# Optimization experiments

Measured on AMD Instinct MI355X. Metric: run time of the kernel, lower is better.

The kernel has to match this reference:

```python
import jax, jax.numpy as jnp
import numpy as np

N = 50000   # nodes per node type
D = 256     # in_dim == out_dim
H = 8       # num heads
DK = D // H # 32
E = 500000  # edges per edge type
LN_EPS = 1e-5


def setup_inputs() -> dict:
    key = jax.random.key(0)
    ks = jax.random.split(key, 16)
    w = lambda k, shape: jax.random.normal(k, shape, dtype=jnp.float32) * 0.05
    xav = np.sqrt(6.0 / (DK + DK))
    return {
        'feats': jax.random.normal(ks[0], (2, N, D), dtype=jnp.float32),
        'Wk': w(ks[1], (2, D, D)), 'bk': jnp.zeros((2, D), jnp.float32),
        'Wq': w(ks[2], (2, D, D)), 'bq': jnp.zeros((2, D), jnp.float32),
        'Wv': w(ks[3], (2, D, D)), 'bv': jnp.zeros((2, D), jnp.float32),
        'Wa': w(ks[4], (2, D, D)), 'ba': jnp.zeros((2, D), jnp.float32),
        'ln_w': jnp.ones((2, D), jnp.float32), 'ln_b': jnp.zeros((2, D), jnp.float32),
        'skip': jnp.ones((2,), jnp.float32),
        'mu': jnp.ones((2, H), jnp.float32),
        'w_att': jax.random.uniform(ks[5], (2, H, DK, DK), jnp.float32, -xav, xav),
        'w_msg': jax.random.uniform(ks[6], (2, H, DK, DK), jnp.float32, -xav, xav),
        'src': jax.random.randint(ks[7], (2, E), 0, N, dtype=jnp.int32),
        'dst': jax.random.randint(ks[8], (2, E), 0, N, dtype=jnp.int32),
    }


def _edge_softmax(scores, seg, n):
    # scores: (E, H); softmax over edges sharing the same destination node
    m = jax.ops.segment_max(scores, seg, num_segments=n)          # (N, H)
    e = jnp.exp(scores - m[seg])
    s = jax.ops.segment_sum(e, seg, num_segments=n)               # (N, H)
    return e / s[seg]


def _forward(feats, Wk, bk, Wq, bq, Wv, bv, Wa, ba, ln_w, ln_b, skip,
             mu, w_att, w_msg, src, dst):
    # canonical etypes: 0 = author->paper, 1 = paper->author
    stypes, dtypes = (0, 1), (1, 0)
    scale = 1.0 / jnp.sqrt(jnp.asarray(DK, feats.dtype))
    h = [None, None]
    for et in range(2):
        st, dt = stypes[et], dtypes[et]
        s_idx, d_idx = src[et], dst[et]
        k = (feats[st] @ Wk[st] + bk[st]).reshape(N, H, DK)
        k = jnp.einsum('nhi,hij->nhj', k, w_att[et])
        v = (feats[st] @ Wv[st] + bv[st]).reshape(N, H, DK)
        v = jnp.einsum('nhi,hij->nhj', v, w_msg[et])
        q = (feats[dt] @ Wq[dt] + bq[dt]).reshape(N, H, DK)
        t = jnp.einsum('ehd,ehd->eh', q[d_idx], k[s_idx])         # (E, H)
        attn = _edge_softmax(t * mu[et] * scale, d_idx, N)        # (E, H)
        msg = v[s_idx] * attn[..., None]                          # (E, H, DK)
        h[dt] = jax.ops.segment_sum(msg, d_idx, num_segments=N).reshape(N, D)
    h = jnp.stack(h)  # (2, N, D); each ntype receives from exactly one etype

    trans = jnp.einsum('tnd,tde->tne', h, Wa) + ba[:, None, :]
    alpha = jax.nn.sigmoid(skip)[:, None, None]
    out = alpha * trans + (1.0 - alpha) * feats
    mean = out.mean(-1, keepdims=True)
    var = out.var(-1, keepdims=True)
    out = (out - mean) * jax.lax.rsqrt(var + LN_EPS)
    return out * ln_w[:, None, :] + ln_b[:, None, :]


def reference(feats, Wk, bk, Wq, bq, Wv, bv, Wa, ba, ln_w, ln_b, skip,
              mu, w_att, w_msg, src, dst):
    return _forward(feats, Wk, bk, Wq, bq, Wv, bv, Wa, ba, ln_w, ln_b, skip,
                    mu, w_att, w_msg, src, dst)
```

## Files before the change

kernel.cpp:

```cpp
#include <hip/hip_runtime.h>
#include <hip/hip_bf16.h>

#define D 256
#define H 8
#define DK 32

typedef unsigned short ushort_t;
typedef unsigned int uint_t;
typedef __attribute__((ext_vector_type(4))) float floatx4;
typedef __attribute__((ext_vector_type(2))) float floatx2;
typedef __attribute__((ext_vector_type(8))) short shortx8;
typedef __attribute__((ext_vector_type(8))) unsigned short ushortx8;

typedef __attribute__((address_space(3))) void lds_void_t;
typedef const __attribute__((address_space(1))) void gbl_void_t;

__device__ __forceinline__ float b2f(ushort_t u) {
    return __uint_as_float(((uint_t)u) << 16);
}
__device__ __forceinline__ floatx2 b2x2(uint_t u) {
    floatx2 r;
    r.x = __uint_as_float(u << 16);
    r.y = __uint_as_float(u & 0xffff0000u);
    return r;
}
__device__ __forceinline__ ushort_t f2b(float f) {
    uint_t u = __float_as_uint(f);
    uint_t r = (u + 0x7FFFu + ((u >> 16) & 1u)) >> 16;
    return (ushort_t)r;
}
__device__ __forceinline__ void async_cp16(const void* g, void* l) {
    __builtin_amdgcn_global_load_lds((gbl_void_t*)g, (lds_void_t*)l, 16, 0, 0);
}

__global__ void cvt_bf16(const float* __restrict__ in, ushort_t* __restrict__ out, size_t n4) {
    size_t i = (size_t)blockIdx.x * blockDim.x + threadIdx.x;
    if (i >= n4) return;
    float4 v = ((const float4*)in)[i];
    ushort4 o;
    o.x = f2b(v.x); o.y = f2b(v.y); o.z = f2b(v.z); o.w = f2b(v.w);
    ((ushort4*)out)[i] = o;
}

__global__ void zero_int(int* __restrict__ p, int n) {
    int i = blockIdx.x * blockDim.x + threadIdx.x;
    if (i < n) p[i] = 0;
}

__global__ void fold_weights(const float* __restrict__ Wk, const float* __restrict__ bk,
                             const float* __restrict__ Wv, const float* __restrict__ bv,
                             const float* __restrict__ w_att, const float* __restrict__ w_msg,
                             float* __restrict__ Wkc, float* __restrict__ bkc,
                             float* __restrict__ Wvc, float* __restrict__ bvc) {
    int r = blockIdx.x, et = blockIdx.y, which = blockIdx.z;
    int tid = threadIdx.x;
    const float* Wsrc = (which ? Wv : Wk) + (size_t)et * D * D + (size_t)r * D;
    const float* wt   = (which ? w_msg : w_att) + (size_t)et * H * DK * DK;
    float* Wdst = (which ? Wvc : Wkc) + (size_t)et * D * D;
    __shared__ float wrow[D];
    wrow[tid] = Wsrc[tid];
    __syncthreads();
    int h = tid >> 5, j = tid & 31;
    const float* wth = wt + h * DK * DK;
    float acc = 0.f;
#pragma unroll 8
    for (int i = 0; i < DK; i++) acc += wrow[h * 32 + i] * wth[i * 32 + j];
    Wdst[(size_t)r * D + tid] = acc;
    if (r == 0) {
        const float* bsrc = (which ? bv : bk) + et * D;
        float* bdst = (which ? bvc : bkc) + et * D;
        float bacc = 0.f;
#pragma unroll 8
        for (int i = 0; i < DK; i++) bacc += bsrc[h * 32 + i] * wth[i * 32 + j];
        bdst[tid] = bacc;
    }
}

__global__ void pack_weights(const float* __restrict__ Wq, const float* __restrict__ bq,
                             const float* __restrict__ Wkc, const float* __restrict__ bkc,
                             const float* __restrict__ Wvc, const float* __restrict__ bvc,
                             const float* __restrict__ Wa,
                             ushort_t* __restrict__ WT_all, ushort_t* __restrict__ WaT,
                             float* __restrict__ bias_all) {
    int idx = blockIdx.x * blockDim.x + threadIdx.x;
    const int NW = 2 * 768 * 256;
    if (idx < NW) {
        int t = idx / (768 * 256);
        int rem = idx - t * 768 * 256;
        int n = rem >> 8, k = rem & 255;
        int sec = n >> 8, nn = n & 255;
        const float* W = (sec == 0) ? Wq : (sec == 1) ? Wkc : Wvc;
        WT_all[idx] = f2b(W[(size_t)t * D * D + (size_t)k * D + nn]);
    } else if (idx < NW + 2 * 256 * 256) {
        int r = idx - NW;
        int t = r / (256 * 256);
        int rem = r - t * 256 * 256;
        int n = rem >> 8, k = rem & 255;
        WaT[r] = f2b(Wa[(size_t)t * D * D + (size_t)k * D + n]);
    }
    if (idx < 2 * 768) {
        int t = idx / 768, n = idx % 768;
        int sec = n >> 8, nn = n & 255;
        const float* b = (sec == 0) ? bq : (sec == 1) ? bkc : bvc;
        bias_all[idx] = b[t * D + nn];
    }
}

#define TM 128
#define TN 128
#define TKK 32
__launch_bounds__(256)
__global__ void gemm_mfma(const ushort_t* __restrict__ A, int lda,
                          const ushort_t* __restrict__ BT,
                          const float* __restrict__ bias,
                          ushort_t* __restrict__ C, int ldc, int M) {
    __shared__ ushort_t As[TM * TKK];
    __shared__ ushort_t Bs[TN * TKK];
    int tid = threadIdx.x;
    int w = tid >> 6, lane = tid & 63;

    int nwg  = gridDim.x * gridDim.y;
    int orig = blockIdx.y * gridDim.x + blockIdx.x;
    int q = nwg >> 3, r = nwg & 7;
    int xcd = orig & 7, loc = orig >> 3;
    int wgid = (xcd < r ? xcd * (q + 1) : r * (q + 1) + (xcd - r) * q) + loc;
    int ncol = gridDim.y;
    int rowt = wgid / ncol;
    int colt = wgid - rowt * ncol;
    int bm = rowt * TM;
    int bn = colt * TN;

    int wm = (w & 1) * 64, wn = (w >> 1) * 64;

    floatx4 acc[4][4] = {};

    int srow = lane >> 2;
    int scol = (lane & 3) * 8;

    for (int kc = 0; kc < 256; kc += TKK) {
#pragma unroll
        for (int j = 0; j < 2; j++) {
            int rr = w * 32 + j * 16;
            int gr = bm + rr + srow; if (gr >= M) gr = M - 1;
            async_cp16(A + (size_t)gr * lda + kc + scol, As + rr * TKK);
            int gn = bn + rr + srow;
            async_cp16(BT + (size_t)gn * 256 + kc + scol, Bs + rr * TKK);
        }
        __builtin_amdgcn_s_waitcnt(0x0F70);
        __syncthreads();

        int fr = lane & 15, fq = lane >> 4;
        shortx8 af[4], bf[4];
#pragma unroll
        for (int i = 0; i < 4; i++)
            af[i] = *(const shortx8*)(As + (wm + i * 16 + fr) * TKK + fq * 8);
#pragma unroll
        for (int j = 0; j < 4; j++)
            bf[j] = *(const shortx8*)(Bs + (wn + j * 16 + fr) * TKK + fq * 8);
#pragma unroll
        for (int i = 0; i < 4; i++)
#pragma unroll
            for (int j = 0; j < 4; j++)
                acc[i][j] = __builtin_amdgcn_mfma_f32_16x16x32_bf16(af[i], bf[j], acc[i][j], 0, 0, 0);
        __syncthreads();
    }

    int fr = lane & 15, fq = lane >> 4;
#pragma unroll
    for (int i = 0; i < 4; i++) {
#pragma unroll
        for (int j = 0; j < 4; j++) {
            int col = bn + wn + j * 16 + fr;
            float bv = bias[col];
#pragma unroll
            for (int rr = 0; rr < 4; rr++) {
                int row = bm + wm + i * 16 + fq * 4 + rr;
                if (row < M) C[(size_t)row * ldc + col] = f2b(acc[i][j][rr] + bv);
            }
        }
    }
}

__global__ void count_deg(const int* __restrict__ dst, int* __restrict__ deg,
                          int N, int E) {
    int i = blockIdx.x * blockDim.x + threadIdx.x;
    if (i >= 2 * E) return;
    int et = i / E, e = i - et * E;
    int d = dst[(size_t)et * E + e];
    atomicAdd(&deg[(1 - et) * N + d], 1);
}

__launch_bounds__(256)
__global__ void scan_blocks(int* __restrict__ deg, int* __restrict__ bsum, int n) {
    __shared__ int wsum[4];
    int tid = threadIdx.x, lane = tid & 63, w = tid >> 6;
    int i = blockIdx.x * 256 + tid;
    int v = (i < n) ? deg[i] : 0;
    int x = v;
#pragma unroll
    for (int off = 1; off < 64; off <<= 1) {
        int y = __shfl_up(x, off);
        if (lane >= off) x += y;
    }
    if (lane == 63) wsum[w] = x;
    __syncthreads();
    int add = 0;
    if (w > 0) add += wsum[0];
    if (w > 1) add += wsum[1];
    if (w > 2) add += wsum[2];
    int incl = x + add;
    if (i < n) deg[i] = incl - v;
    if (tid == 255) bsum[blockIdx.x] = incl;
}

__launch_bounds__(512)
__global__ void scan_tops(int* __restrict__ bsum, int* __restrict__ row_ptr,
                          int nb, int n) {
    __shared__ int wsum[8];
    int tid = threadIdx.x, lane = tid & 63, w = tid >> 6;
    int v = (tid < nb) ? bsum[tid] : 0;
    int x = v;
#pragma unroll
    for (int off = 1; off < 64; off <<= 1) {
        int y = __shfl_up(x, off);
        if (lane >= off) x += y;
    }
    if (lane == 63) wsum[w] = x;
    __syncthreads();
    int add = 0;
    for (int j = 0; j < w; j++) add += wsum[j];
    int incl = x + add;
    if (tid < nb) bsum[tid] = incl - v;
    if (tid == nb - 1) row_ptr[n] = incl;
}

__launch_bounds__(256)
__global__ void scan_apply(const int* __restrict__ excl, const int* __restrict__ bsum,
                           int* __restrict__ row_ptr, int* __restrict__ cursor, int n) {
    int i = blockIdx.x * 256 + threadIdx.x;
    if (i >= n) return;
    int e = excl[i] + bsum[blockIdx.x];
    row_ptr[i] = e;
    cursor[i] = e;
}

__global__ void fill_edges(const int* __restrict__ src, const int* __restrict__ dst,
                           int* __restrict__ cursor, int* __restrict__ ebuf,
                           int N, int E) {
    int i = blockIdx.x * blockDim.x + threadIdx.x;
    if (i >= 2 * E) return;
    int et = i / E, e = i - et * E;
    int d = dst[(size_t)et * E + e];
    int s = src[(size_t)et * E + e];
    int pos = atomicAdd(&cursor[(1 - et) * N + d], 1);
    ebuf[pos] = s;
}

__launch_bounds__(256)
__global__ void node_aggregate(ushort_t* __restrict__ QKV, const float* __restrict__ mu,
                               const int* __restrict__ row_ptr, const int* __restrict__ ebuf,
                               int N) {
    int wid = (blockIdx.x * blockDim.x + threadIdx.x) >> 6;
    int lane = threadIdx.x & 63;
    if (wid >= 2 * N) return;
    int dt = (wid >= N) ? 1 : 0;
    int et = 1 - dt;
    int l = lane & 31;
    int half = lane >> 5;
    int h = l >> 2;

    uint4 qu = ((const uint4*)(QKV + (size_t)wid * 768))[l];
    floatx2 q01 = b2x2(qu.x), q23 = b2x2(qu.y), q45 = b2x2(qu.z), q67 = b2x2(qu.w);
    float sc = mu[et * H + h] * 0.17677669529663687f;
    int beg = row_ptr[wid], end = row_ptr[wid + 1];
    const ushort_t* KVb = QKV + (size_t)et * N * 768;

    floatx2 a01 = {0.f, 0.f}, a23 = {0.f, 0.f}, a45 = {0.f, 0.f}, a67 = {0.f, 0.f};
    float ssum = 0.f;

    int idx = beg + half;
    uint4 ku0 = {}, vu0 = {};
    int s1v = 0;
    if (idx < end) {
        int s0v = ebuf[idx];
        int i2 = idx + 2;
        s1v = ebuf[i2 < end ? i2 : idx];
        const ushort_t* srow = KVb + (size_t)s0v * 768 + l * 8;
        ku0 = *(const uint4*)(srow + 256);
        vu0 = *(const uint4*)(srow + 512);
    }
    while (idx < end) {
        int i2 = idx + 2;
        uint4 ku1 = ku0, vu1 = vu0;
        int s2v = s1v;
        if (i2 < end) {
            int i4 = idx + 4;
            s2v = ebuf[i4 < end ? i4 : i2];
            const ushort_t* srow = KVb + (size_t)s1v * 768 + l * 8;
            ku1 = *(const uint4*)(srow + 256);
            vu1 = *(const uint4*)(srow + 512);
        }
        floatx2 pv = q01 * b2x2(ku0.x);
        pv += q23 * b2x2(ku0.y);
        pv += q45 * b2x2(ku0.z);
        pv += q67 * b2x2(ku0.w);
        float p = pv.x + pv.y;
        p += __shfl_xor(p, 1);
        p += __shfl_xor(p, 2);
        float ex = __expf(p * sc);
        ssum += ex;
        floatx2 ex2 = {ex, ex};
        a01 += ex2 * b2x2(vu0.x);
        a23 += ex2 * b2x2(vu0.y);
        a45 += ex2 * b2x2(vu0.z);
        a67 += ex2 * b2x2(vu0.w);
        ku0 = ku1; vu0 = vu1; s1v = s2v;
        idx = i2;
    }
    ssum += __shfl_xor(ssum, 32);
    a01.x += __shfl_xor(a01.x, 32); a01.y += __shfl_xor(a01.y, 32);
    a23.x += __shfl_xor(a23.x, 32); a23.y += __shfl_xor(a23.y, 32);
    a45.x += __shfl_xor(a45.x, 32); a45.y += __shfl_xor(a45.y, 32);
    a67.x += __shfl_xor(a67.x, 32); a67.y += __shfl_xor(a67.y, 32);
    float r = (ssum > 0.f) ? 1.0f / ssum : 0.0f;
    if (half == 0) {
        ushortx8 hv;
        hv[0] = f2b(a01.x * r); hv[1] = f2b(a01.y * r);
        hv[2] = f2b(a23.x * r); hv[3] = f2b(a23.y * r);
        hv[4] = f2b(a45.x * r); hv[5] = f2b(a45.y * r);
        hv[6] = f2b(a67.x * r); hv[7] = f2b(a67.y * r);
        ((ushortx8*)(QKV + (size_t)wid * 768))[l] = hv;
    }
}

__launch_bounds__(256)
__global__ void skip_ln(const ushort_t* __restrict__ trans, const float* __restrict__ feats,
                        const float* __restrict__ lnw, const float* __restrict__ lnb,
                        const float* __restrict__ skip, float* __restrict__ out, int N) {
    int wid = (blockIdx.x * blockDim.x + threadIdx.x) >> 6;
    int lane = threadIdx.x & 63;
    if (wid >= 2 * N) return;
    int t = (wid >= N) ? 1 : 0;
    float alpha = 1.0f / (1.0f + __expf(-skip[t]));
    float beta = 1.0f - alpha;
    size_t base = (size_t)wid * D;
    ushort4 tu = ((const ushort4*)(trans + base))[lane];
    float4 fu = ((const float4*)(feats + base))[lane];
    float x0 = alpha * b2f(tu.x) + beta * fu.x;
    float x1 = alpha * b2f(tu.y) + beta * fu.y;
    float x2 = alpha * b2f(tu.z) + beta * fu.z;
    float x3 = alpha * b2f(tu.w) + beta * fu.w;
    float s  = x0 + x1 + x2 + x3;
    float sq = x0 * x0 + x1 * x1 + x2 * x2 + x3 * x3;
#pragma unroll
    for (int off = 1; off < 64; off <<= 1) {
        s  += __shfl_xor(s,  off);
        sq += __shfl_xor(sq, off);
    }
    float mean = s * (1.0f / 256.0f);
    float var  = sq * (1.0f / 256.0f) - mean * mean;
    float r = rsqrtf(var + 1e-5f);
    float4 w4 = ((const float4*)(lnw + t * D))[lane];
    float4 b4 = ((const float4*)(lnb + t * D))[lane];
    float4 o;
    o.x = (x0 - mean) * r * w4.x + b4.x;
    o.y = (x1 - mean) * r * w4.y + b4.y;
    o.z = (x2 - mean) * r * w4.z + b4.z;
    o.w = (x3 - mean) * r * w4.w + b4.w;
    ((float4*)(out + base))[lane] = o;
}

extern "C" void kernel_launch(void* const* d_in, const int* in_sizes, int n_in,
                              void* d_out, int out_size, void* d_ws, size_t ws_size,
                              hipStream_t stream) {
    const float* feats = (const float*)d_in[0];
    const float* Wk    = (const float*)d_in[1];
    const float* bk    = (const float*)d_in[2];
    const float* Wq    = (const float*)d_in[3];
    const float* bq    = (const float*)d_in[4];
    const float* Wv    = (const float*)d_in[5];
    const float* bv    = (const float*)d_in[6];
    const float* Wa    = (const float*)d_in[7];
    const float* ba    = (const float*)d_in[8];
    const float* ln_w  = (const float*)d_in[9];
    const float* ln_b  = (const float*)d_in[10];
    const float* skip  = (const float*)d_in[11];
    const float* mu    = (const float*)d_in[12];
    const float* w_att = (const float*)d_in[13];
    const float* w_msg = (const float*)d_in[14];
    const int*   src   = (const int*)d_in[15];
    const int*   dst   = (const int*)d_in[16];
    float* out = (float*)d_out;

    const int N = in_sizes[0] / (2 * D);
    const int E = in_sizes[15] / 2;
    const int NN = 2 * N;
    const size_t ND2 = 2 * (size_t)N * D;

    float* ws = (float*)d_ws;
    size_t off = 0;
    float* Wkc  = ws + off; off += 2 * (size_t)D * D;
    float* Wvc  = ws + off; off += 2 * (size_t)D * D;
    float* bkc  = ws + off; off += 2 * D;
    float* bvc  = ws + off; off += 2 * D;
    float* bias_all = ws + off; off += 2 * 768;
    ushort_t* WT_all = (ushort_t*)(ws + off); off += 2 * 768 * 256 / 2;
    ushort_t* WaT    = (ushort_t*)(ws + off); off += 2 * 256 * 256 / 2;
    ushort_t* featsb = (ushort_t*)(ws + off); off += ND2 / 2;
    ushort_t* QKV    = (ushort_t*)(ws + off); off += 2 * (size_t)N * 768 / 2;
    int* deg     = (int*)(ws + off); off += NN;
    int* row_ptr = (int*)(ws + off); off += NN + 1;
    int* cursor  = (int*)(ws + off); off += NN + 1;
    int* ebuf    = (int*)(ws + off); off += 2 * (size_t)E;
    int* bsum    = (int*)(ws + off); off += 512;

    const int nb = (NN + 255) / 256;

    zero_int<<<(NN + 255) / 256, 256, 0, stream>>>(deg, NN);
    count_deg<<<(2 * E + 255) / 256, 256, 0, stream>>>(dst, deg, N, E);
    scan_blocks<<<nb, 256, 0, stream>>>(deg, bsum, NN);
    scan_tops<<<1, 512, 0, stream>>>(bsum, row_ptr, nb, NN);
    scan_apply<<<nb, 256, 0, stream>>>(deg, bsum, row_ptr, cursor, NN);
    fill_edges<<<(2 * E + 255) / 256, 256, 0, stream>>>(src, dst, cursor, ebuf, N, E);

    fold_weights<<<dim3(D, 2, 2), 256, 0, stream>>>(Wk, bk, Wv, bv, w_att, w_msg,
                                                    Wkc, bkc, Wvc, bvc);
    pack_weights<<<(2 * 768 * 256 + 2 * 256 * 256 + 255) / 256, 256, 0, stream>>>(
        Wq, bq, Wkc, bkc, Wvc, bvc, Wa, WT_all, WaT, bias_all);

    cvt_bf16<<<(unsigned)((ND2 / 4 + 255) / 256), 256, 0, stream>>>(feats, featsb, ND2 / 4);

    dim3 qkv_grid((N + TM - 1) / TM, 768 / TN);
    for (int t = 0; t < 2; t++)
        gemm_mfma<<<qkv_grid, 256, 0, stream>>>(featsb + (size_t)t * N * D, D,
                                                WT_all + (size_t)t * 768 * 256,
                                                bias_all + t * 768,
                                                QKV + (size_t)t * N * 768, 768, N);

    node_aggregate<<<(NN * 64 + 255) / 256, 256, 0, stream>>>(QKV, mu, row_ptr, ebuf, N);

    ushort_t* transb = featsb;
    dim3 tr_grid((N + TM - 1) / TM, 256 / TN);
    for (int t = 0; t < 2; t++)
        gemm_mfma<<<tr_grid, 256, 0, stream>>>(QKV + (size_t)t * N * 768, 768,
                                               WaT + (size_t)t * 256 * 256,
                                               ba + t * 256,
                                               transb + (size_t)t * N * D, D, N);

    skip_ln<<<(NN * 64 + 255) / 256, 256, 0, stream>>>(transb, feats, ln_w, ln_b, skip, out, N);
}
```

Measured before the change: 633.3 us.

## Widen GEMM K-tile with swizzled LDS, batch type launches, deepen gather prefetch

The GEMM K-tile grows from 32 to 64. Global-to-LDS copies use an XOR swizzle on 16-byte column groups to avoid bank conflicts, and there are half as many barrier rounds. The two per-type GEMM launches are merged into one launch with blockIdx.z picking the type, which removes launch gaps and gives a larger grid. The aggregation loop now keeps two edges in flight per half-wave, which adds register pressure in exchange for more hidden gather latency.

```diff
diff --git a/kernel.cpp b/kernel.cpp
--- a/kernel.cpp
+++ b/kernel.cpp
@@ -108,16 +108,21 @@
 
 #define TM 128
 #define TN 128
-#define TKK 32
+#define TKK 64
 __launch_bounds__(256)
-__global__ void gemm_mfma(const ushort_t* __restrict__ A, int lda,
-                          const ushort_t* __restrict__ BT,
-                          const float* __restrict__ bias,
-                          ushort_t* __restrict__ C, int ldc, int M) {
+__global__ void gemm_mfma(const ushort_t* __restrict__ A0, int lda, size_t aStr,
+                          const ushort_t* __restrict__ BT0, size_t bStr,
+                          const float* __restrict__ bias0, int biasStr,
+                          ushort_t* __restrict__ C0, int ldc, size_t cStr, int M) {
     __shared__ ushort_t As[TM * TKK];
     __shared__ ushort_t Bs[TN * TKK];
     int tid = threadIdx.x;
     int w = tid >> 6, lane = tid & 63;
+    int t = blockIdx.z;
+    const ushort_t* A  = A0 + (size_t)t * aStr;
+    const ushort_t* BT = BT0 + (size_t)t * bStr;
+    const float* bias  = bias0 + (size_t)t * biasStr;
+    ushort_t* C        = C0 + (size_t)t * cStr;
 
     int nwg  = gridDim.x * gridDim.y;
     int orig = blockIdx.y * gridDim.x + blockIdx.x;
@@ -134,38 +139,44 @@
 
     floatx4 acc[4][4] = {};
 
-    int srow = lane >> 2;
-    int scol = (lane & 3) * 8;
+    int sr8    = lane >> 3;
+    int swzcol = 8 * ((lane & 7) ^ sr8);
+
+    int fr = lane & 15, fq = lane >> 4;
+    int fswz = (fr & 7) * 8;
 
     for (int kc = 0; kc < 256; kc += TKK) {
 #pragma unroll
-        for (int j = 0; j < 2; j++) {
-            int rr = w * 32 + j * 16;
-            int gr = bm + rr + srow; if (gr >= M) gr = M - 1;
-            async_cp16(A + (size_t)gr * lda + kc + scol, As + rr * TKK);
-            int gn = bn + rr + srow;
-            async_cp16(BT + (size_t)gn * 256 + kc + scol, Bs + rr * TKK);
+        for (int j = 0; j < 4; j++) {
+            int rr = w * 32 + j * 8;
+            int gr = bm + rr + sr8; if (gr >= M) gr = M - 1;
+            async_cp16(A + (size_t)gr * lda + kc + swzcol, As + rr * TKK);
+            int gn = bn + rr + sr8;
+            async_cp16(BT + (size_t)gn * 256 + kc + swzcol, Bs + rr * TKK);
         }
         __builtin_amdgcn_s_waitcnt(0x0F70);
         __syncthreads();
 
-        int fr = lane & 15, fq = lane >> 4;
-        shortx8 af[4], bf[4];
-#pragma unroll
-        for (int i = 0; i < 4; i++)
-            af[i] = *(const shortx8*)(As + (wm + i * 16 + fr) * TKK + fq * 8);
-#pragma unroll
-        for (int j = 0; j < 4; j++)
-            bf[j] = *(const shortx8*)(Bs + (wn + j * 16 + fr) * TKK + fq * 8);
-#pragma unroll
-        for (int i = 0; i < 4; i++)
+#pragma unroll
+        for (int kk = 0; kk < 2; kk++) {
+            shortx8 af[4], bf[4];
+            int rcol = (kk * 32) ^ fswz;
+#pragma unroll
+            for (int i = 0; i < 4; i++)
+                af[i] = *(const shortx8*)(As + (wm + i * 16 + fr) * TKK + ((kk * 32 + fq * 8) ^ fswz));
 #pragma unroll
             for (int j = 0; j < 4; j++)
-                acc[i][j] = __builtin_amdgcn_mfma_f32_16x16x32_bf16(af[i], bf[j], acc[i][j], 0, 0, 0);
+                bf[j] = *(const shortx8*)(Bs + (wn + j * 16 + fr) * TKK + ((kk * 32 + fq * 8) ^ fswz));
+#pragma unroll
+            for (int i = 0; i < 4; i++)
+#pragma unroll
+                for (int j = 0; j < 4; j++)
+                    acc[i][j] = __builtin_amdgcn_mfma_f32_16x16x32_bf16(af[i], bf[j], acc[i][j], 0, 0, 0);
+            (void)rcol;
+        }
         __syncthreads();
     }
 
-    int fr = lane & 15, fq = lane >> 4;
 #pragma unroll
     for (int i = 0; i < 4; i++) {
 #pragma unroll
@@ -273,50 +284,72 @@
     floatx2 q01 = b2x2(qu.x), q23 = b2x2(qu.y), q45 = b2x2(qu.z), q67 = b2x2(qu.w);
     float sc = mu[et * H + h] * 0.17677669529663687f;
     int beg = row_ptr[wid], end = row_ptr[wid + 1];
-    const ushort_t* KVb = QKV + (size_t)et * N * 768;
+    const ushort_t* KVb = QKV + (size_t)et * N * 768 + l * 8;
 
     floatx2 a01 = {0.f, 0.f}, a23 = {0.f, 0.f}, a45 = {0.f, 0.f}, a67 = {0.f, 0.f};
     float ssum = 0.f;
 
-    int idx = beg + half;
-    uint4 ku0 = {}, vu0 = {};
-    int s1v = 0;
-    if (idx < end) {
-        int s0v = ebuf[idx];
-        int i2 = idx + 2;
-        s1v = ebuf[i2 < end ? i2 : idx];
-        const ushort_t* srow = KVb + (size_t)s0v * 768 + l * 8;
-        ku0 = *(const uint4*)(srow + 256);
-        vu0 = *(const uint4*)(srow + 512);
-    }
-    while (idx < end) {
-        int i2 = idx + 2;
-        uint4 ku1 = ku0, vu1 = vu0;
-        int s2v = s1v;
-        if (i2 < end) {
-            int i4 = idx + 4;
-            s2v = ebuf[i4 < end ? i4 : i2];
-            const ushort_t* srow = KVb + (size_t)s1v * 768 + l * 8;
-            ku1 = *(const uint4*)(srow + 256);
-            vu1 = *(const uint4*)(srow + 512);
+#define AGG_COMPUTE(kk, vv)                                              \
+    {                                                                    \
+        floatx2 pv = q01 * b2x2(kk.x);                                   \
+        pv += q23 * b2x2(kk.y);                                          \
+        pv += q45 * b2x2(kk.z);                                          \
+        pv += q67 * b2x2(kk.w);                                          \
+        float pp = pv.x + pv.y;                                          \
+        pp += __shfl_xor(pp, 1);                                         \
+        pp += __shfl_xor(pp, 2);                                         \
+        float ex = __expf(pp * sc);                                      \
+        ssum += ex;                                                      \
+        floatx2 e2 = {ex, ex};                                           \
+        a01 += e2 * b2x2(vv.x);                                          \
+        a23 += e2 * b2x2(vv.y);                                          \
+        a45 += e2 * b2x2(vv.z);                                          \
+        a67 += e2 * b2x2(vv.w);                                          \
+    }
+
+    int p = beg + half;
+    uint4 kA = {}, vA = {}, kB = {}, vB = {};
+    int sC = 0, sD = 0;
+    if (p < end) {
+        int sA = ebuf[p];
+        const ushort_t* r0 = KVb + (size_t)sA * 768;
+        kA = *(const uint4*)(r0 + 256);
+        vA = *(const uint4*)(r0 + 512);
+        sC = (p + 4 < end) ? ebuf[p + 4] : sA;
+    }
+    if (p + 2 < end) {
+        int sB = ebuf[p + 2];
+        const ushort_t* r1 = KVb + (size_t)sB * 768;
+        kB = *(const uint4*)(r1 + 256);
+        vB = *(const uint4*)(r1 + 512);
+        sD = (p + 6 < end) ? ebuf[p + 6] : sB;
+    }
+    while (p < end) {
+        uint4 nk = kA, nv = vA;
+        int sE = sC;
+        if (p + 4 < end) {
+            const ushort_t* rr = KVb + (size_t)sC * 768;
+            nk = *(const uint4*)(rr + 256);
+            nv = *(const uint4*)(rr + 512);
+            if (p + 8 < end) sE = ebuf[p + 8];
         }
-        floatx2 pv = q01 * b2x2(ku0.x);
-        pv += q23 * b2x2(ku0.y);
-        pv += q45 * b2x2(ku0.z);
-        pv += q67 * b2x2(ku0.w);
-        float p = pv.x + pv.y;
-        p += __shfl_xor(p, 1);
-        p += __shfl_xor(p, 2);
-        float ex = __expf(p * sc);
-        ssum += ex;
-        floatx2 ex2 = {ex, ex};
-        a01 += ex2 * b2x2(vu0.x);
-        a23 += ex2 * b2x2(vu0.y);
-        a45 += ex2 * b2x2(vu0.z);
-        a67 += ex2 * b2x2(vu0.w);
-        ku0 = ku1; vu0 = vu1; s1v = s2v;
-        idx = i2;
-    }
+        AGG_COMPUTE(kA, vA);
+        kA = nk; vA = nv; sC = sE;
+        p += 2;
+        if (p >= end) break;
+        nk = kB; nv = vB; sE = sD;
+        if (p + 4 < end) {
+            const ushort_t* rr = KVb + (size_t)sD * 768;
+            nk = *(const uint4*)(rr + 256);
+            nv = *(const uint4*)(rr + 512);
+            if (p + 8 < end) sE = ebuf[p + 8];
+        }
+        AGG_COMPUTE(kB, vB);
+        kB = nk; vB = nv; sD = sE;
+        p += 2;
+    }
+#undef AGG_COMPUTE
+
     ssum += __shfl_xor(ssum, 32);
     a01.x += __shfl_xor(a01.x, 32); a01.y += __shfl_xor(a01.y, 32);
     a23.x += __shfl_xor(a23.x, 32); a23.y += __shfl_xor(a23.y, 32);
@@ -430,22 +463,20 @@
 
     cvt_bf16<<<(unsigned)((ND2 / 4 + 255) / 256), 256, 0, stream>>>(feats, featsb, ND2 / 4);
 
-    dim3 qkv_grid((N + TM - 1) / TM, 768 / TN);
-    for (int t = 0; t < 2; t++)
-        gemm_mfma<<<qkv_grid, 256, 0, stream>>>(featsb + (size_t)t * N * D, D,
-                                                WT_all + (size_t)t * 768 * 256,
-                                                bias_all + t * 768,
-                                                QKV + (size_t)t * N * 768, 768, N);
+    dim3 qkv_grid((N + TM - 1) / TM, 768 / TN, 2);
+    gemm_mfma<<<qkv_grid, 256, 0, stream>>>(featsb, D, (size_t)N * D,
+                                            WT_all, (size_t)768 * 256,
+                                            bias_all, 768,
+                                            QKV, 768, (size_t)N * 768, N);
 
     node_aggregate<<<(NN * 64 + 255) / 256, 256, 0, stream>>>(QKV, mu, row_ptr, ebuf, N);
 
     ushort_t* transb = featsb;
-    dim3 tr_grid((N + TM - 1) / TM, 256 / TN);
-    for (int t = 0; t < 2; t++)
-        gemm_mfma<<<tr_grid, 256, 0, stream>>>(QKV + (size_t)t * N * 768, 768,
-                                               WaT + (size_t)t * 256 * 256,
-                                               ba + t * 256,
-                                               transb + (size_t)t * N * D, D, N);
+    dim3 tr_grid((N + TM - 1) / TM, 256 / TN, 2);
+    gemm_mfma<<<tr_grid, 256, 0, stream>>>(QKV, 768, (size_t)N * 768,
+                                           WaT, (size_t)256 * 256,
+                                           ba, 256,
+                                           transb, D, (size_t)N * D, N);
 
     skip_ln<<<(NN * 64 + 255) / 256, 256, 0, stream>>>(transb, feats, ln_w, ln_b, skip, out, N);
 }
```

Result: no change. 622.0 us (-1.8%).
